# Optimization experiments

Measured on AMD Instinct MI355X. Metric: run time of the kernel, lower is better.

Reference implementation:

```python
import jax, jax.numpy as jnp
import numpy as np

B, S, DIM, H, DH = 1, 4096, 1536, 12, 128
EPS = 1e-6


def _rmsnorm(x, w):
    # RMSNorm over last dim (inner_dim), elementwise affine
    var = jnp.mean(x * x, axis=-1, keepdims=True)
    return x * jax.lax.rsqrt(var + EPS) * w


def _apply_rope(x, freqs_cos, freqs_sin):
    # x: [B, S, H, DH]; freqs: [1, S, 1, DH] interleaved layout
    x1 = x[..., 0::2]
    x2 = x[..., 1::2]
    cos = freqs_cos[..., 0::2]
    sin = freqs_sin[..., 1::2]
    o1 = x1 * cos - x2 * sin
    o2 = x1 * sin + x2 * cos
    return jnp.stack([o1, o2], axis=-1).reshape(x.shape)


def setup_inputs() -> dict:
    key = jax.random.key(0)
    ks = jax.random.split(key, 4)
    # realistic interleaved rotary freqs
    pos = jnp.arange(S, dtype=jnp.float32)[:, None]
    inv = 1.0 / (10000.0 ** (jnp.arange(0, DH, 2, dtype=jnp.float32) / DH))
    ang = jnp.repeat(pos * inv, 2, axis=-1)  # [S, DH] interleaved
    freqs_cos = jnp.cos(ang)[None, :, None, :]
    freqs_sin = jnp.sin(ang)[None, :, None, :]
    return {
        "hidden_states": jax.random.normal(ks[0], (B, S, DIM), jnp.float32),
        "w_qkv": jax.random.normal(ks[1], (3 * DIM, DIM), jnp.float32) * 0.02,
        "b_qkv": jnp.zeros((3 * DIM,), jnp.float32),
        "norm_q_w": jnp.ones((DIM,), jnp.float32),
        "norm_k_w": jnp.ones((DIM,), jnp.float32),
        "w_out": jax.random.normal(ks[2], (DIM, DIM), jnp.float32) * 0.02,
        "b_out": jnp.zeros((DIM,), jnp.float32),
        "freqs_cos": freqs_cos,
        "freqs_sin": freqs_sin,
    }


def reference(hidden_states, w_qkv, b_qkv, norm_q_w, norm_k_w, w_out, b_out,
              freqs_cos, freqs_sin):
    # fused QKV projection (dequantized-equivalent of SVDQW4A4Linear)
    qkv = jnp.einsum("bsd,fd->bsf", hidden_states, w_qkv) + b_qkv  # [B,S,3*DIM]
    q, k, v = jnp.split(qkv, 3, axis=-1)
    # qk RMSNorm over inner_dim
    q = _rmsnorm(q, norm_q_w)
    k = _rmsnorm(k, norm_k_w)
    # split heads -> [B, S, H, DH]
    q = q.reshape(B, S, H, DH)
    k = k.reshape(B, S, H, DH)
    v = v.reshape(B, S, H, DH)
    # rotary embedding on q, k
    q = _apply_rope(q, freqs_cos, freqs_sin)
    k = _apply_rope(k, freqs_cos, freqs_sin)
    # scaled dot-product attention
    scale = 1.0 / jnp.sqrt(jnp.float32(DH))
    scores = jnp.einsum("bqhd,bkhd->bhqk", q, k) * scale  # [B,H,S,S]
    probs = jax.nn.softmax(scores, axis=-1)
    attn = jnp.einsum("bhqk,bkhd->bqhd", probs, v)  # [B,S,H,DH]
    attn = attn.reshape(B, S, DIM)
    # output projection (dropout is identity at inference)
    return jnp.einsum("bsd,fd->bsf", attn, w_out) + b_out
```

## Files before the change

### kernel.cpp

```cpp
#include <hip/hip_runtime.h>
#include <stdint.h>

typedef unsigned short u16;
typedef __bf16 bf16x8 __attribute__((ext_vector_type(8)));
typedef __bf16 bf16x4 __attribute__((ext_vector_type(4)));
typedef unsigned short u16x4 __attribute__((ext_vector_type(4)));
typedef unsigned short u16x8 __attribute__((ext_vector_type(8)));
typedef float f32x4 __attribute__((ext_vector_type(4)));

#define SEQ 4096
#define DMODEL 1536
#define NHEAD 12
#define DHEAD 128

__device__ __forceinline__ u16 f2bf(float f) {
  union { float f; uint32_t u; } cv;
  cv.f = f;
  uint32_t u = cv.u + 0x7FFFu + ((cv.u >> 16) & 1u);
  return (u16)(u >> 16);
}

__device__ __forceinline__ float bf2f(u16 u) {
  union { uint32_t u; float f; } cv;
  cv.u = ((uint32_t)u) << 16;
  return cv.f;
}

__device__ __forceinline__ f32x4 mfma16(bf16x8 a, bf16x8 b, f32x4 c) {
  return __builtin_amdgcn_mfma_f32_16x16x32_bf16(a, b, c, 0, 0, 0);
}

typedef unsigned char __attribute__((address_space(1))) gas_byte;
typedef unsigned char __attribute__((address_space(3))) las_byte;

__device__ __forceinline__ void gld_lds16(const void* g, void* l) {
  __builtin_amdgcn_global_load_lds((gas_byte*)g, (las_byte*)l, 16, 0, 0);
}

__global__ __launch_bounds__(256) void k_cvt3(const float* __restrict__ a, u16* __restrict__ oa, int na,
                                              const float* __restrict__ b, u16* __restrict__ ob, int nb,
                                              const float* __restrict__ c, u16* __restrict__ oc, int nc) {
  int i = blockIdx.x * 256 + threadIdx.x;
  const float* src;
  u16* dst;
  int off;
  if (i < na) { src = a; dst = oa; off = i; }
  else if (i < na + nb) { src = b; dst = ob; off = i - na; }
  else if (i < na + nb + nc) { src = c; dst = oc; off = i - na - nb; }
  else return;
  float4 v = reinterpret_cast<const float4*>(src)[off];
  u16x4 o;
  o.x = f2bf(v.x); o.y = f2bf(v.y); o.z = f2bf(v.z); o.w = f2bf(v.w);
  reinterpret_cast<u16x4*>(dst)[off] = o;
}

template <bool BF16OUT>
__global__ __launch_bounds__(256, 3) void k_gemm_bt(const u16* __restrict__ A, const u16* __restrict__ B,
                                                    const float* __restrict__ bias, void* __restrict__ Cv,
                                                    int M, int N, int K) {
  __shared__ u16 As[128 * 64];
  __shared__ u16 Bs[192 * 64];
  const int t = threadIdx.x;
  const int w = t >> 6, l = t & 63;
  const int lr = l & 15, lh = l >> 4;
  const int wr = w >> 1, wc = w & 1;

  int id = blockIdx.y * gridDim.x + blockIdx.x;
  const int nwg = gridDim.x * gridDim.y;
  id = (id & 7) * (nwg >> 3) + (id >> 3);
  const int bn = id % gridDim.x, bm = id / gridDim.x;

  const u16* Ag = A + (size_t)bm * 128 * K + (size_t)(t >> 3) * K + (t & 7) * 8;
  const u16* Bg = B + (size_t)bn * 192 * K + (size_t)(t >> 3) * K + (t & 7) * 8;
  u16* Asw = As + t * 8;
  u16* Bsw = Bs + t * 8;

  f32x4 acc[4][6];
#pragma unroll
  for (int i = 0; i < 4; ++i)
#pragma unroll
    for (int j = 0; j < 6; ++j)
      acc[i][j] = (f32x4){0.f, 0.f, 0.f, 0.f};

  for (int kt = 0; kt < K; kt += 64) {
#pragma unroll
    for (int it = 0; it < 4; ++it)
      gld_lds16(Ag + (size_t)it * 32 * K + kt, Asw + it * 2048);
#pragma unroll
    for (int it = 0; it < 6; ++it)
      gld_lds16(Bg + (size_t)it * 32 * K + kt, Bsw + it * 2048);
    __syncthreads();
#pragma unroll
    for (int kk = 0; kk < 2; ++kk) {
      const int koff = kk * 32 + lh * 8;
      bf16x8 af[4], bfv[6];
#pragma unroll
      for (int mf = 0; mf < 4; ++mf)
        af[mf] = *reinterpret_cast<const bf16x8*>(As + (wr * 64 + mf * 16 + lr) * 64 + koff);
#pragma unroll
      for (int nf = 0; nf < 6; ++nf)
        bfv[nf] = *reinterpret_cast<const bf16x8*>(Bs + (wc * 96 + nf * 16 + lr) * 64 + koff);
#pragma unroll
      for (int mf = 0; mf < 4; ++mf)
#pragma unroll
        for (int nf = 0; nf < 6; ++nf)
          acc[mf][nf] = mfma16(af[mf], bfv[nf], acc[mf][nf]);
    }
    __syncthreads();
  }

  const size_t row0 = (size_t)bm * 128 + wr * 64;
  const int col0 = bn * 192 + wc * 96;
#pragma unroll
  for (int mf = 0; mf < 4; ++mf)
#pragma unroll
    for (int i = 0; i < 4; ++i) {
      const size_t r = row0 + mf * 16 + lh * 4 + i;
#pragma unroll
      for (int nf = 0; nf < 6; ++nf) {
        const int c = nf * 16 + lr;
        const float vv = acc[mf][nf][i] + bias[col0 + c];
        if constexpr (BF16OUT)
          ((u16*)Cv)[r * N + col0 + c] = f2bf(vv);
        else
          ((float*)Cv)[r * N + col0 + c] = vv;
      }
    }
}

__global__ __launch_bounds__(256) void k_normrope(const u16* __restrict__ qkvb,
    const float* __restrict__ nqw, const float* __restrict__ nkw,
    const float* __restrict__ fcos, const float* __restrict__ fsin,
    u16* __restrict__ qh, u16* __restrict__ kh, u16* __restrict__ vh) {
  const int s = blockIdx.x;
  const int t = threadIdx.x;
  const u16* row = qkvb + (size_t)s * (3 * DMODEL);
  const float QSCALE = 0.08838834764831845f * 1.4426950408889634f;

  float2 qv[3], kvv[3];
  float ssq = 0.f, ssk = 0.f;
#pragma unroll
  for (int r = 0; r < 3; ++r) {
    const int d = 2 * (t + 256 * r);
    uint32_t aw = *reinterpret_cast<const uint32_t*>(row + d);
    uint32_t bw = *reinterpret_cast<const uint32_t*>(row + DMODEL + d);
    qv[r].x  = bf2f((u16)aw); qv[r].y  = bf2f((u16)(aw >> 16));
    kvv[r].x = bf2f((u16)bw); kvv[r].y = bf2f((u16)(bw >> 16));
    ssq += qv[r].x * qv[r].x + qv[r].y * qv[r].y;
    ssk += kvv[r].x * kvv[r].x + kvv[r].y * kvv[r].y;
  }
#pragma unroll
  for (int off = 32; off > 0; off >>= 1) {
    ssq += __shfl_down(ssq, off);
    ssk += __shfl_down(ssk, off);
  }
  __shared__ float red[8];
  const int w = t >> 6, l = t & 63;
  if (l == 0) { red[w] = ssq; red[4 + w] = ssk; }
  __syncthreads();
  const float rq = rsqrtf((red[0] + red[1] + red[2] + red[3]) * (1.f / DMODEL) + 1e-6f);
  const float rk = rsqrtf((red[4] + red[5] + red[6] + red[7]) * (1.f / DMODEL) + 1e-6f);

#pragma unroll
  for (int r = 0; r < 3; ++r) {
    const int P = t + 256 * r;
    const int d = 2 * P;
    const int hh = P >> 6;
    const int dh = (P & 63) * 2;
    const float c  = fcos[s * DHEAD + dh];
    const float si = fsin[s * DHEAD + dh + 1];
    const size_t ob = ((size_t)hh * SEQ + s) * DHEAD + dh;
    float x1 = qv[r].x * rq * nqw[d];
    float x2 = qv[r].y * rq * nqw[d + 1];
    qh[ob]     = f2bf((x1 * c - x2 * si) * QSCALE);
    qh[ob + 1] = f2bf((x1 * si + x2 * c) * QSCALE);
    x1 = kvv[r].x * rk * nkw[d];
    x2 = kvv[r].y * rk * nkw[d + 1];
    kh[ob]     = f2bf(x1 * c - x2 * si);
    kh[ob + 1] = f2bf(x1 * si + x2 * c);
    vh[ob]     = row[2 * DMODEL + d];
    vh[ob + 1] = row[2 * DMODEL + d + 1];
  }
}

__global__ __launch_bounds__(256) void k_transpose_v(const u16* __restrict__ vh, u16* __restrict__ vt) {
  const int h = blockIdx.x >> 6;
  const int st = blockIdx.x & 63;
  __shared__ u16 tile[64][136];
  const int t = threadIdx.x;
  const u16* src = vh + ((size_t)h * SEQ + st * 64) * DHEAD;
#pragma unroll
  for (int p = 0; p < 8; ++p) {
    const int r = p * 8 + (t >> 5);
    const int c = (t & 31) * 4;
    u16x4 v = *reinterpret_cast<const u16x4*>(src + (size_t)r * DHEAD + c);
    *reinterpret_cast<u16x4*>(&tile[r][c]) = v;
  }
  __syncthreads();
  u16* dst = vt + (size_t)h * DHEAD * SEQ + st * 64;
#pragma unroll
  for (int p = 0; p < 8; ++p) {
    const int d = p * 16 + (t >> 4);
    const int s4 = (t & 15) * 4;
    u16x4 v;
    v.x = tile[s4][d]; v.y = tile[s4 + 1][d]; v.z = tile[s4 + 2][d]; v.w = tile[s4 + 3][d];
    *reinterpret_cast<u16x4*>(dst + (size_t)d * SEQ + s4) = v;
  }
}

__global__ __launch_bounds__(256, 3) void k_attn(const u16* __restrict__ qh, const u16* __restrict__ kh,
                                                 const u16* __restrict__ vt,
                                                 u16* __restrict__ po, float* __restrict__ pl) {
  int bid = blockIdx.y * 64 + blockIdx.x;
  bid = (bid & 7) * 96 + (bid >> 3);
  const int h = bid >> 6;
  const int rest = bid & 63;
  const int sp = rest >> 5;
  const int qg = rest & 31;

  const int tx = threadIdx.x;
  const int w = tx >> 6, l = tx & 63;
  const int lr = l & 15, lh = l >> 4;
  const int q0 = qg * 128 + w * 32;

  __shared__ u16 S[25600];
  u16* Pw = S + 20480 + w * 1280;

  const u16* Q  = qh + ((size_t)h * SEQ + q0) * DHEAD;
  const u16* Kh = kh + (size_t)h * SEQ * DHEAD;
  const u16* Vh = vt + (size_t)h * DHEAD * SEQ;

  int kOff[2], vOff[2];
#pragma unroll
  for (int it = 0; it < 2; ++it) {
    const int g = it * 256 + tx;
    const int krow = g >> 4, kc = g & 15;
    kOff[it] = krow * 128 + ((kc ^ (krow & 7)) * 8);
    const int vrow = g >> 2, vc = g & 3;
    vOff[it] = vrow * 4096 + ((vc ^ ((vrow >> 1) & 3)) * 8);
  }

  const u16* kp[4];
#pragma unroll
  for (int kk = 0; kk < 4; ++kk)
    kp[kk] = S + lr * 128 + (((kk * 4 + lh) ^ (lr & 7)) * 8);
  const int vlane = lr * 32 + ((lh ^ ((lr >> 1) & 3)) * 8);
  const u16* prd = Pw + lr * 40 + lh * 8;
  u16* pwr = Pw + lr * 40 + lh * 4;

  bf16x8 aq[2][4];
#pragma unroll
  for (int mf = 0; mf < 2; ++mf)
#pragma unroll
    for (int kk = 0; kk < 4; ++kk)
      aq[mf][kk] = *reinterpret_cast<const bf16x8*>(Q + (size_t)(mf * 16 + lr) * DHEAD + kk * 32 + lh * 8);

  bf16x8 vone;
#pragma unroll
  for (int j = 0; j < 8; ++j) vone[j] = (__bf16)1.0f;

  f32x4 o[2][9];
#pragma unroll
  for (int mf = 0; mf < 2; ++mf)
#pragma unroll
    for (int nd = 0; nd < 9; ++nd)
      o[mf][nd] = (f32x4){0.f, 0.f, 0.f, 0.f};

  const int kv0 = sp * (SEQ / 2);

#define STAGE_T(kvt, kdst, vdst)                                         \
  {                                                                      \
    const u16* kg_ = Kh + (size_t)(kvt) * 128;                           \
    const u16* vg_ = Vh + (kvt);                                         \
    gld_lds16(kg_ + kOff[0], S + (kdst) + tx * 8);                       \
    gld_lds16(kg_ + kOff[1], S + (kdst) + 2048 + tx * 8);                \
    gld_lds16(vg_ + vOff[0], S + 8192 + (vdst) + tx * 8);                \
    gld_lds16(vg_ + vOff[1], S + 8192 + (vdst) + 2048 + tx * 8);         \
  }

#define QK_T(kc)                                                                      \
  {                                                                                   \
    sc[0][0] = sc[0][1] = sc[1][0] = sc[1][1] = (f32x4){0.f, 0.f, 0.f, 0.f};          \
    __builtin_amdgcn_s_setprio(1);                                                    \
    _Pragma("unroll")                                                                 \
    for (int nf = 0; nf < 2; ++nf) {                                                  \
      _Pragma("unroll")                                                               \
      for (int kk = 0; kk < 4; ++kk) {                                                \
        bf16x8 bk = *reinterpret_cast<const bf16x8*>(kp[kk] + (kc) + nf * 2048);      \
        sc[0][nf] = mfma16(bk, aq[0][kk], sc[0][nf]);                                 \
        sc[1][nf] = mfma16(bk, aq[1][kk], sc[1][nf]);                                 \
      }                                                                               \
    }                                                                                 \
    __builtin_amdgcn_s_setprio(0);                                                    \
  }

#define PV_T(vo)                                                                      \
  {                                                                                   \
    bf16x8 bp0 = *reinterpret_cast<const bf16x8*>(prd);                               \
    bf16x8 bp1 = *reinterpret_cast<const bf16x8*>(prd + 640);                         \
    __builtin_amdgcn_s_setprio(1);                                                    \
    o[0][8] = mfma16(vone, bp0, o[0][8]);                                             \
    o[1][8] = mfma16(vone, bp1, o[1][8]);                                             \
    _Pragma("unroll")                                                                 \
    for (int nd = 0; nd < 8; ++nd) {                                                  \
      bf16x8 av = *reinterpret_cast<const bf16x8*>(S + 8192 + (vo) + vlane + nd * 512); \
      o[0][nd] = mfma16(av, bp0, o[0][nd]);                                           \
      o[1][nd] = mfma16(av, bp1, o[1][nd]);                                           \
    }                                                                                 \
    __builtin_amdgcn_s_setprio(0);                                                    \
  }

#define EXPWR_T()                                                                     \
  {                                                                                   \
    _Pragma("unroll")                                                                 \
    for (int mf = 0; mf < 2; ++mf) {                                                  \
      _Pragma("unroll")                                                               \
      for (int nf = 0; nf < 2; ++nf) {                                                \
        bf16x4 pk;                                                                    \
        pk[0] = (__bf16)exp2f(sc[mf][nf][0]);                                         \
        pk[1] = (__bf16)exp2f(sc[mf][nf][1]);                                         \
        pk[2] = (__bf16)exp2f(sc[mf][nf][2]);                                         \
        pk[3] = (__bf16)exp2f(sc[mf][nf][3]);                                         \
        *reinterpret_cast<bf16x4*>(pwr + mf * 640 + nf * 16) = pk;                    \
      }                                                                               \
    }                                                                                 \
  }

  f32x4 sc[2][2];

  STAGE_T(kv0, 0, 0)
  __syncthreads();

  int kcur = 0;
  int vprev = 8192, vcur = 0, vnext = 4096;

  STAGE_T(kv0 + 32, 4096, 4096)
  QK_T(0)
  EXPWR_T()
  __syncthreads();
  kcur = 4096; vprev = 0; vcur = 4096; vnext = 8192;

  for (int tt = 1; tt < 64; ++tt) {
    if (tt < 63)
      STAGE_T(kv0 + (tt + 1) * 32, kcur ^ 4096, vnext)
    QK_T(kcur)
    PV_T(vprev)
    EXPWR_T()
    __syncthreads();
    kcur ^= 4096;
    const int vtmp = vprev; vprev = vcur; vcur = vnext; vnext = vtmp;
  }
  PV_T(vprev)

#undef STAGE_T
#undef QK_T
#undef PV_T
#undef EXPWR_T

  const size_t hb = (size_t)(sp * NHEAD + h) * SEQ;
#pragma unroll
  for (int mf = 0; mf < 2; ++mf) {
    const int q = q0 + mf * 16 + lr;
    const float lsum = o[mf][8][0];
    const float inv = 1.f / lsum;
    u16* orow = po + (hb + q) * 128 + lh * 4;
#pragma unroll
    for (int nd = 0; nd < 8; ++nd) {
      bf16x4 v4;
      v4[0] = (__bf16)(o[mf][nd][0] * inv);
      v4[1] = (__bf16)(o[mf][nd][1] * inv);
      v4[2] = (__bf16)(o[mf][nd][2] * inv);
      v4[3] = (__bf16)(o[mf][nd][3] * inv);
      *reinterpret_cast<bf16x4*>(orow + nd * 16) = v4;
    }
    if (lh == 0)
      pl[hb + q] = lsum;
  }
}

__global__ __launch_bounds__(256) void k_combine(const u16* __restrict__ po,
                                                 const float* __restrict__ pl, u16* __restrict__ attnb) {
  const int i = blockIdx.x * 256 + threadIdx.x;
  const int hs = i >> 4, c8 = i & 15;
  const int h = hs >> 12, s = hs & 4095;
  const float l0 = pl[hs], l1 = pl[49152 + hs];
  const float inv = 1.f / (l0 + l1);
  const float w0 = l0 * inv, w1 = l1 * inv;
  u16x8 a = *reinterpret_cast<const u16x8*>(po + (size_t)hs * 128 + c8 * 8);
  u16x8 b = *reinterpret_cast<const u16x8*>(po + ((size_t)49152 + hs) * 128 + c8 * 8);
  u16x8 o;
#pragma unroll
  for (int j = 0; j < 8; ++j)
    o[j] = f2bf(w0 * bf2f(a[j]) + w1 * bf2f(b[j]));
  *reinterpret_cast<u16x8*>(attnb + (size_t)s * DMODEL + h * DHEAD + c8 * 8) = o;
}

extern "C" void kernel_launch(void* const* d_in, const int* in_sizes, int n_in,
                              void* d_out, int out_size, void* d_ws, size_t ws_size,
                              hipStream_t stream) {
  const float* x     = (const float*)d_in[0];
  const float* w_qkv = (const float*)d_in[1];
  const float* b_qkv = (const float*)d_in[2];
  const float* nqw   = (const float*)d_in[3];
  const float* nkw   = (const float*)d_in[4];
  const float* w_out = (const float*)d_in[5];
  const float* b_out = (const float*)d_in[6];
  const float* fcos  = (const float*)d_in[7];
  const float* fsin  = (const float*)d_in[8];
  float* out = (float*)d_out;
  char* ws = (char*)d_ws;

  u16* qkvb  = (u16*)(ws);
  u16* po    = (u16*)(ws);
  float* pl  = (float*)(ws + 50331648);
  u16* attnb = (u16*)(ws + 51118080);
  u16* qh  = (u16*)(ws + 75497472);
  u16* kh  = (u16*)(ws + 88080384);
  u16* vh  = (u16*)(ws + 100663296);
  u16* vt  = (u16*)(ws + 113246208);
  u16* xb  = (u16*)(ws + 125829120);
  u16* wqb = (u16*)(ws + 138412032);
  u16* wob = (u16*)(ws + 152567808);

  k_cvt3<<<15360, 256, 0, stream>>>(x, xb, 1572864, w_qkv, wqb, 1769472, w_out, wob, 589824);
  k_gemm_bt<true><<<dim3(24, 32), 256, 0, stream>>>(xb, wqb, b_qkv, qkvb, 4096, 4608, 1536);
  k_normrope<<<4096, 256, 0, stream>>>(qkvb, nqw, nkw, fcos, fsin, qh, kh, vh);
  k_transpose_v<<<768, 256, 0, stream>>>(vh, vt);
  k_attn<<<dim3(64, 12), 256, 0, stream>>>(qh, kh, vt, po, pl);
  k_combine<<<3072, 256, 0, stream>>>(po, pl, attnb);
  k_gemm_bt<false><<<dim3(8, 32), 256, 0, stream>>>(attnb, wob, b_out, out, 4096, 1536, 1536);
}
```

Baseline: 275.3 us.

## Double-buffer GEMM K-tiles with swizzled LDS and use native exp2 in attention

Restructures the QKV/output GEMM main loop to use two 32-wide K LDS buffers. The next tile's global-to-LDS loads are issued before the current tile's MFMAs, leaving one barrier per step. The LDS layout gets an XOR swizzle on the 8-element chunk index to cut bank conflicts on fragment reads. Separately, the attention softmax exponent now calls the hardware exp2 builtin instead of exp2f, which drops denormal/range handling. Risks include less work per barrier with the smaller K-tile and relying on hardware exp2 precision.

```diff
diff --git a/kernel.cpp b/kernel.cpp
--- a/kernel.cpp
+++ b/kernel.cpp
@@ -58,8 +58,8 @@
 __global__ __launch_bounds__(256, 3) void k_gemm_bt(const u16* __restrict__ A, const u16* __restrict__ B,
                                                     const float* __restrict__ bias, void* __restrict__ Cv,
                                                     int M, int N, int K) {
-  __shared__ u16 As[128 * 64];
-  __shared__ u16 Bs[192 * 64];
+  __shared__ u16 As[2][128 * 32];
+  __shared__ u16 Bs[2][192 * 32];
   const int t = threadIdx.x;
   const int w = t >> 6, l = t & 63;
   const int lr = l & 15, lh = l >> 4;
@@ -70,10 +70,20 @@
   id = (id & 7) * (nwg >> 3) + (id >> 3);
   const int bn = id % gridDim.x, bm = id / gridDim.x;
 
-  const u16* Ag = A + (size_t)bm * 128 * K + (size_t)(t >> 3) * K + (t & 7) * 8;
-  const u16* Bg = B + (size_t)bn * 192 * K + (size_t)(t >> 3) * K + (t & 7) * 8;
-  u16* Asw = As + t * 8;
-  u16* Bsw = Bs + t * 8;
+  size_t aOff[2];
+  size_t bOff[3];
+#pragma unroll
+  for (int it = 0; it < 2; ++it) {
+    const int g = it * 256 + t;
+    aOff[it] = (size_t)(g >> 2) * K + (size_t)(((g & 3) ^ ((g >> 2) & 3)) * 8);
+  }
+#pragma unroll
+  for (int it = 0; it < 3; ++it) {
+    const int g = it * 256 + t;
+    bOff[it] = (size_t)(g >> 2) * K + (size_t)(((g & 3) ^ ((g >> 2) & 3)) * 8);
+  }
+  const u16* Ag = A + (size_t)bm * 128 * K;
+  const u16* Bg = B + (size_t)bn * 192 * K;
 
   f32x4 acc[4][6];
 #pragma unroll
@@ -82,32 +92,53 @@
     for (int j = 0; j < 6; ++j)
       acc[i][j] = (f32x4){0.f, 0.f, 0.f, 0.f};
 
-  for (int kt = 0; kt < K; kt += 64) {
-#pragma unroll
-    for (int it = 0; it < 4; ++it)
-      gld_lds16(Ag + (size_t)it * 32 * K + kt, Asw + it * 2048);
-#pragma unroll
-    for (int it = 0; it < 6; ++it)
-      gld_lds16(Bg + (size_t)it * 32 * K + kt, Bsw + it * 2048);
+  int aRd[4], bRd[6];
+#pragma unroll
+  for (int mf = 0; mf < 4; ++mf) {
+    const int row = wr * 64 + mf * 16 + lr;
+    aRd[mf] = row * 32 + ((lh ^ (lr & 3)) * 8);
+  }
+#pragma unroll
+  for (int nf = 0; nf < 6; ++nf) {
+    const int row = wc * 96 + nf * 16 + lr;
+    bRd[nf] = row * 32 + ((lh ^ (lr & 3)) * 8);
+  }
+
+#define G_STAGE(kt, buf)                                                  \
+  {                                                                       \
+    const u16* a_ = Ag + (size_t)(kt) * 32;                               \
+    const u16* b_ = Bg + (size_t)(kt) * 32;                               \
+    gld_lds16(a_ + aOff[0], &As[buf][t * 8]);                             \
+    gld_lds16(a_ + aOff[1], &As[buf][2048 + t * 8]);                      \
+    gld_lds16(b_ + bOff[0], &Bs[buf][t * 8]);                             \
+    gld_lds16(b_ + bOff[1], &Bs[buf][2048 + t * 8]);                      \
+    gld_lds16(b_ + bOff[2], &Bs[buf][4096 + t * 8]);                      \
+  }
+
+  const int NKT = K >> 5;
+  G_STAGE(0, 0)
+  __syncthreads();
+
+  int buf = 0;
+  for (int kt = 0; kt < NKT; ++kt) {
+    if (kt + 1 < NKT)
+      G_STAGE(kt + 1, buf ^ 1)
+    bf16x8 af[4], bfv[6];
+#pragma unroll
+    for (int mf = 0; mf < 4; ++mf)
+      af[mf] = *reinterpret_cast<const bf16x8*>(&As[buf][aRd[mf]]);
+#pragma unroll
+    for (int nf = 0; nf < 6; ++nf)
+      bfv[nf] = *reinterpret_cast<const bf16x8*>(&Bs[buf][bRd[nf]]);
+#pragma unroll
+    for (int mf = 0; mf < 4; ++mf)
+#pragma unroll
+      for (int nf = 0; nf < 6; ++nf)
+        acc[mf][nf] = mfma16(af[mf], bfv[nf], acc[mf][nf]);
     __syncthreads();
-#pragma unroll
-    for (int kk = 0; kk < 2; ++kk) {
-      const int koff = kk * 32 + lh * 8;
-      bf16x8 af[4], bfv[6];
-#pragma unroll
-      for (int mf = 0; mf < 4; ++mf)
-        af[mf] = *reinterpret_cast<const bf16x8*>(As + (wr * 64 + mf * 16 + lr) * 64 + koff);
-#pragma unroll
-      for (int nf = 0; nf < 6; ++nf)
-        bfv[nf] = *reinterpret_cast<const bf16x8*>(Bs + (wc * 96 + nf * 16 + lr) * 64 + koff);
-#pragma unroll
-      for (int mf = 0; mf < 4; ++mf)
-#pragma unroll
-        for (int nf = 0; nf < 6; ++nf)
-          acc[mf][nf] = mfma16(af[mf], bfv[nf], acc[mf][nf]);
-    }
-    __syncthreads();
-  }
+    buf ^= 1;
+  }
+#undef G_STAGE
 
   const size_t row0 = (size_t)bm * 128 + wr * 64;
   const int col0 = bn * 192 + wc * 96;
@@ -317,10 +348,10 @@
       _Pragma("unroll")                                                               \
       for (int nf = 0; nf < 2; ++nf) {                                                \
         bf16x4 pk;                                                                    \
-        pk[0] = (__bf16)exp2f(sc[mf][nf][0]);                                         \
-        pk[1] = (__bf16)exp2f(sc[mf][nf][1]);                                         \
-        pk[2] = (__bf16)exp2f(sc[mf][nf][2]);                                         \
-        pk[3] = (__bf16)exp2f(sc[mf][nf][3]);                                         \
+        pk[0] = (__bf16)__builtin_amdgcn_exp2f(sc[mf][nf][0]);                        \
+        pk[1] = (__bf16)__builtin_amdgcn_exp2f(sc[mf][nf][1]);                        \
+        pk[2] = (__bf16)__builtin_amdgcn_exp2f(sc[mf][nf][2]);                        \
+        pk[3] = (__bf16)__builtin_amdgcn_exp2f(sc[mf][nf][3]);                        \
         *reinterpret_cast<bf16x4*>(pwr + mf * 640 + nf * 16) = pk;                    \
       }                                                                               \
     }                                                                                 \
```

Measured after the change: 265.2 us. 1.04x faster.
